# Kernel tuning notes

Measured on AMD Instinct MI355X. Metric: run time of the kernel, lower is better.

## Reference

```python
import jax, jax.numpy as jnp
import numpy as np

N_E = 16384
E_DIM = 64
GROUPS = 4
N_E_GROUP = N_E // GROUPS  # 4096
B, H, W = 16, 32, 32


def _l2norm(x):
    # matches F.normalize(p=2, dim=-1) with eps=1e-12
    n = jnp.linalg.norm(x, axis=-1, keepdims=True)
    return x / jnp.maximum(n, 1e-12)


def setup_inputs() -> dict:
    key = jax.random.key(0)
    k1, k2 = jax.random.split(key)
    z_groups = jax.random.normal(k1, (B, GROUPS * E_DIM, H, W), dtype=jnp.float32)
    emb = jax.random.uniform(k2, (N_E, E_DIM), minval=-1.0 / N_E, maxval=1.0 / N_E,
                             dtype=jnp.float32)
    emb = _l2norm(emb)  # module normalizes codebook at init when l2_norm=True
    return {"z_groups": z_groups, "embedding": emb}


def reference(z_groups, embedding):
    # Eval-mode forward (no EMA/random-restart buffer updates, losses are 0).
    b, c, h, w = z_groups.shape
    # split channels into groups: b (g*c) h w -> b h w g c
    z = z_groups.reshape(b, GROUPS, E_DIM, h, w).transpose(0, 3, 4, 1, 2)
    z = _l2norm(z)                                     # l2_norm=True path
    zf = z.reshape(-1, GROUPS, E_DIM)                  # [N, g, c]
    emb = _l2norm(embedding.reshape(GROUPS, N_E_GROUP, E_DIM))  # [g, k, c]

    # d = -|z|^2 - |e|^2 + 2 z.e  (negative squared distance), argmax = nearest
    d = (2.0 * jnp.einsum('ngc,gkc->ngk', zf, emb)
         - jnp.sum(zf * zf, axis=-1)[..., None]
         - jnp.sum(emb * emb, axis=-1)[None, :, :])    # [N, g, k]
    idx = jnp.argmax(d, axis=-1)                       # [N, g]

    zq = emb[jnp.arange(GROUPS)[None, :], idx]         # [N, g, c] gather
    zq = zf + jax.lax.stop_gradient(zq - zf)           # straight-through

    # b h w g c -> b (g*c) h w
    quant = zq.reshape(b, h, w, GROUPS, E_DIM).transpose(0, 3, 4, 1, 2)
    quant = quant.reshape(b, GROUPS * E_DIM, h, w)

    vq_loss = jnp.zeros((GROUPS,), jnp.float32)
    commit_loss = jnp.zeros((GROUPS,), jnp.float32)
    codebook_usage = jnp.zeros((GROUPS,), jnp.float32)

    # perplexity / min_encodings correspond to the last group (loop semantics)
    min_encodings = jax.nn.one_hot(idx[:, -1], N_E_GROUP, dtype=quant.dtype)
    avg_probs = jnp.mean(min_encodings, axis=0)
    perplexity = jnp.exp(-jnp.sum(avg_probs * jnp.log(avg_probs + 1e-10)))

    return (quant, vq_loss, commit_loss, codebook_usage,
            perplexity, min_encodings, idx)
```

## Files before the change

kernel.cpp:

```cpp
#include <hip/hip_runtime.h>
#include <hip/hip_bf16.h>
#include <math.h>

#define N_E      16384
#define E_DIM    64
#define GROUPS   4
#define N_E_G    4096
#define NQ       16384

#define OFF_QUANT   0L
#define OFF_VQLOSS  4194304L
#define OFF_PERP    4194316L
#define OFF_MINENC  4194317L
#define OFF_IDX     71303181L

#define WS_EN     0L
#define WS_EN2    1048576L
#define WS_ENHI   1064960L
#define WS_HIST   7880704L
#define WS_IDX3   7884800L

typedef float  float4v  __attribute__((ext_vector_type(4)));
typedef short  short8   __attribute__((ext_vector_type(8)));

static __device__ __forceinline__ ushort f2bf(float x) {
    union { __hip_bfloat16 h; ushort u; } cv; cv.h = __float2bfloat16(x);
    return cv.u;
}

__global__ void norm_emb_kernel(const float* __restrict__ emb,
                                float* __restrict__ en, float* __restrict__ en2,
                                ushort* __restrict__ ehi,
                                int* __restrict__ hist) {
    const int t    = threadIdx.x;
    const int lane = t & 63;
    const int wv   = t >> 6;

    if (blockIdx.x < 16) hist[blockIdx.x * 256 + t] = 0;

    #pragma unroll
    for (int it = 0; it < 4; ++it) {
        int code = blockIdx.x * 16 + wv * 4 + it;
        float x = emb[code * 64 + lane];
        float ss = x * x;
        #pragma unroll
        for (int off = 32; off; off >>= 1) ss += __shfl_xor(ss, off, 64);
        float v = x / fmaxf(sqrtf(ss), 1e-12f);
        en[code * 64 + lane]  = v;
        ehi[code * 64 + lane] = f2bf(v);
        float s2 = v * v;
        #pragma unroll
        for (int off = 32; off; off >>= 1) s2 += __shfl_xor(s2, off, 64);
        if (lane == 0) en2[code] = s2;
    }
}

#define CAP  64
#define TAU  0.017f
#define ZSTR 68

__global__ __launch_bounds__(256, 2)
void vq_cand_kernel(const float* __restrict__ z,
                    const ushort* __restrict__ ehi,
                    const float* __restrict__ en,
                    const float* __restrict__ en2, float* __restrict__ out,
                    int* __restrict__ hist, int* __restrict__ idx3) {
    __shared__ float zn[128 * ZSTR];
    __shared__ float rden[128];
    __shared__ union {
        float tile[64 * 129];
        struct {
            ushort cand[128 * CAP];
            int    cnt[128];
            int    bks[128];
        } kl;
    } sh;

    const int g  = blockIdx.y;
    const int q0 = blockIdx.x * 128;
    const int t  = threadIdx.x;
    const int wave = t >> 6, lane = t & 63;
    const int l15 = lane & 15, quad = lane >> 4;
    const int qhalf = wave & 1, chalf = wave >> 1;

    const int sliceId = blockIdx.y * (NQ / 128) + blockIdx.x;
    float4v* fill4 = (float4v*)(out + OFF_VQLOSS) + (size_t)sliceId * 32768;

    const ushort* abase = ehi + (size_t)g * N_E_G * 64
                        + (size_t)(chalf * 64 + l15) * 64 + quad * 8;
    short8 afA[4][2], afB[4][2];
    #pragma unroll
    for (int cs = 0; cs < 4; ++cs)
        #pragma unroll
        for (int ks = 0; ks < 2; ++ks)
            afA[cs][ks] = *(const short8*)(abase + (size_t)(cs * 16) * 64 + ks * 32);

    {
        const int b = q0 >> 10, hw0 = q0 & 1023;
        const float* src = z + (size_t)b * 262144 + (size_t)g * 65536 + hw0;
        for (int i = t; i < 8192; i += 256) {
            int d = i >> 7, nq = i & 127;
            sh.tile[d * 129 + nq] = src[(size_t)d * 1024 + nq];
        }
        __syncthreads();
        if (t < 128) {
            float ss = 0.f;
            for (int d = 0; d < 64; ++d) {
                float x = sh.tile[d * 129 + t];
                ss = fmaf(x, x, ss);
            }
            rden[t] = fmaxf(sqrtf(ss), 1e-12f);
        }
        __syncthreads();
        for (int i = t; i < 8192; i += 256) {
            int q = i >> 6, d = i & 63;
            zn[q * ZSTR + d] = sh.tile[d * 129 + q] / rden[q];
        }
        __syncthreads();
    }

    if (t < 128) sh.kl.cnt[t] = 0;

    short8 bfrag[4][2];
    #pragma unroll
    for (int uu = 0; uu < 4; ++uu) {
        int ql = qhalf * 64 + uu * 16 + l15;
        #pragma unroll
        for (int ks = 0; ks < 2; ++ks) {
            const float* p = &zn[ql * ZSTR + ks * 32 + quad * 8];
            float4v a = *(const float4v*)p;
            float4v c = *(const float4v*)(p + 4);
            short8 f;
            f[0] = (short)f2bf(a[0]); f[1] = (short)f2bf(a[1]);
            f[2] = (short)f2bf(a[2]); f[3] = (short)f2bf(a[3]);
            f[4] = (short)f2bf(c[0]); f[5] = (short)f2bf(c[1]);
            f[6] = (short)f2bf(c[2]); f[7] = (short)f2bf(c[3]);
            bfrag[uu][ks] = f;
        }
    }
    __syncthreads();

    float Mrun[4];
    #pragma unroll
    for (int u = 0; u < 4; ++u) Mrun[u] = -3.4e38f;

    auto do_tile = [&](short8 (&A)[4][2], short8 (&P)[4][2], int tile) {
        if (tile + 1 < 32) {
            const ushort* p = abase + (size_t)((tile + 1) * 128) * 64;
            #pragma unroll
            for (int cs = 0; cs < 4; ++cs)
                #pragma unroll
                for (int ks = 0; ks < 2; ++ks)
                    P[cs][ks] = *(const short8*)(p + (size_t)(cs * 16) * 64 + ks * 32);
        }
        {
            const float4v z4 = {0.f, 0.f, 0.f, 0.f};
            #pragma unroll
            for (int r = 0; r < 4; ++r)
                __builtin_nontemporal_store(
                    z4, &fill4[(size_t)(tile * 4 + r) * 256 + t]);
        }
        float4v acc[4][4];
        #pragma unroll
        for (int cs = 0; cs < 4; ++cs)
            #pragma unroll
            for (int u = 0; u < 4; ++u) {
                float4v zz = {0.f, 0.f, 0.f, 0.f};
                float4v tmp = __builtin_amdgcn_mfma_f32_16x16x32_bf16(
                                  A[cs][0], bfrag[u][0], zz, 0, 0, 0);
                acc[cs][u] = __builtin_amdgcn_mfma_f32_16x16x32_bf16(
                                  A[cs][1], bfrag[u][1], tmp, 0, 0, 0);
            }
        const int j0 = tile * 128;
        #pragma unroll
        for (int u = 0; u < 4; ++u) {
            float m0 = fmaxf(fmaxf(acc[0][u][0], acc[0][u][1]),
                             fmaxf(acc[0][u][2], acc[0][u][3]));
            float m1 = fmaxf(fmaxf(acc[1][u][0], acc[1][u][1]),
                             fmaxf(acc[1][u][2], acc[1][u][3]));
            float m2 = fmaxf(fmaxf(acc[2][u][0], acc[2][u][1]),
                             fmaxf(acc[2][u][2], acc[2][u][3]));
            float m3 = fmaxf(fmaxf(acc[3][u][0], acc[3][u][1]),
                             fmaxf(acc[3][u][2], acc[3][u][3]));
            float m  = fmaxf(fmaxf(m0, m1), fmaxf(m2, m3));
            float mh = fmaxf(m,  __shfl_xor(m,  16, 64));
            float mw = fmaxf(mh, __shfl_xor(mh, 32, 64));
            Mrun[u] = fmaxf(Mrun[u], mw);
            float thr = Mrun[u] - TAU;
            if (m >= thr) {
                int ql = qhalf * 64 + u * 16 + l15;
                #pragma unroll
                for (int cs = 0; cs < 4; ++cs)
                    #pragma unroll
                    for (int r = 0; r < 4; ++r)
                        if (acc[cs][u][r] >= thr) {
                            int cidx = j0 + chalf * 64 + cs * 16 + quad * 4 + r;
                            int slot = atomicAdd(&sh.kl.cnt[ql], 1);
                            if (slot < CAP) sh.kl.cand[ql * CAP + slot] = (ushort)cidx;
                        }
            }
        }
    };

    for (int tt = 0; tt < 32; tt += 2) {
        do_tile(afA, afB, tt);
        do_tile(afB, afA, tt + 1);
    }

    if (sliceId == 0 && t < 13) out[OFF_VQLOSS + 67108864L + t] = 0.f;
    __syncthreads();

    if (t < 128) {
        int q = q0 + t;
        float za[64];
        const float4v* zp = (const float4v*)(&zn[t * ZSTR]);
        #pragma unroll
        for (int i = 0; i < 16; ++i) {
            float4v v = zp[i];
            za[i*4+0] = v[0]; za[i*4+1] = v[1]; za[i*4+2] = v[2]; za[i*4+3] = v[3];
        }
        int nc = sh.kl.cnt[t]; if (nc > CAP) nc = CAP;
        float best = -3.4e38f; int bk = 0x7fffffff;
        for (int s = 0; s < nc; ++s) {
            int c = sh.kl.cand[t * CAP + s];
            const float* ev = en + ((size_t)g * N_E_G + c) * 64;
            float a = 0.f;
            #pragma unroll
            for (int k = 0; k < 64; ++k) a = fmaf(za[k], ev[k], a);
            float d = 2.f * a - en2[g * N_E_G + c];
            if (d > best || (d == best && c < bk)) { best = d; bk = c; }
        }
        if (bk == 0x7fffffff) bk = 0;
        sh.kl.bks[t] = bk;
        out[OFF_IDX + (size_t)q * 4 + g] = (float)bk;
        if (g == 3) {
            idx3[q] = bk;
            atomicAdd(&hist[bk], 1);
        }
    }
    __syncthreads();

    for (int i = t; i < 128 * 64; i += 256) {
        int d = i >> 7, m = i & 127;
        int n = q0 + m, b = n >> 10, hw = n & 1023;
        float v = en[((size_t)g * N_E_G + sh.kl.bks[m]) * 64 + d];
        __builtin_nontemporal_store(
            v, &out[OFF_QUANT + (size_t)b * 262144 + (size_t)(g * 64 + d) * 1024 + hw]);
    }
}

__global__ void finalize_kernel(const int* __restrict__ idx3,
                                const int* __restrict__ hist,
                                float* __restrict__ out) {
    if (blockIdx.x < 64) {
        int r = blockIdx.x * 256 + threadIdx.x;
        out[OFF_MINENC + (size_t)r * N_E_G + idx3[r]] = 1.0f;
        return;
    }
    __shared__ float s[256];
    int t = threadIdx.x;
    float acc = 0.f;
    for (int k = t; k < N_E_G; k += 256) {
        float p = (float)hist[k] * (1.0f / 16384.0f);
        acc += p * logf(p + 1e-10f);
    }
    s[t] = acc;
    __syncthreads();
    for (int o = 128; o; o >>= 1) {
        if (t < o) s[t] += s[t + o];
        __syncthreads();
    }
    if (t == 0) out[OFF_PERP] = expf(-s[0]);
}

extern "C" void kernel_launch(void* const* d_in, const int* in_sizes, int n_in,
                              void* d_out, int out_size, void* d_ws, size_t ws_size,
                              hipStream_t stream) {
    const float* z_groups = (const float*)d_in[0];
    const float* emb      = (const float*)d_in[1];
    float* out = (float*)d_out;
    float* ws  = (float*)d_ws;

    float*  en   = ws + WS_EN;
    float*  en2  = ws + WS_EN2;
    ushort* ehi  = (ushort*)(ws + WS_ENHI);
    int*    hist = (int*)(ws + WS_HIST);
    int*    idx3 = (int*)(ws + WS_IDX3);

    norm_emb_kernel<<<1024, 256, 0, stream>>>(emb, en, en2, ehi, hist);

    vq_cand_kernel<<<dim3(NQ / 128, GROUPS), 256, 0, stream>>>(
        z_groups, ehi, en, en2, out, hist, idx3);

    finalize_kernel<<<65, 256, 0, stream>>>(idx3, hist, out);
}
```

Measured before the change: 388.9 us.

## Double block size to 512 threads and split candidate rescoring across four slices

Raises the candidate kernel to 512 threads (8 waves), so each wave covers 32 codes per tile instead of 64, which halves the per-wave MFMA accumulators and A-fragment registers. The fp32 rescoring of candidates is split into four strided slices per query, followed by a shared-memory reduction, so more threads work on that serial tail. The intent is higher occupancy and less idle time in the exact-scoring phase. The cost is an extra barrier and extra shared memory, and a launch bound of 4 blocks of 512 may force register spills.

```diff
diff --git a/kernel.cpp b/kernel.cpp
--- a/kernel.cpp
+++ b/kernel.cpp
@@ -59,7 +59,7 @@
 #define TAU  0.017f
 #define ZSTR 68
 
-__global__ __launch_bounds__(256, 2)
+__global__ __launch_bounds__(512, 4)
 void vq_cand_kernel(const float* __restrict__ z,
                     const ushort* __restrict__ ehi,
                     const float* __restrict__ en,
@@ -73,6 +73,8 @@
             ushort cand[128 * CAP];
             int    cnt[128];
             int    bks[128];
+            float  bestd[512];
+            int    bestk[512];
         } kl;
     } sh;
 
@@ -81,16 +83,16 @@
     const int t  = threadIdx.x;
     const int wave = t >> 6, lane = t & 63;
     const int l15 = lane & 15, quad = lane >> 4;
-    const int qhalf = wave & 1, chalf = wave >> 1;
+    const int qhalf = wave & 1, cquad = wave >> 1;
 
     const int sliceId = blockIdx.y * (NQ / 128) + blockIdx.x;
     float4v* fill4 = (float4v*)(out + OFF_VQLOSS) + (size_t)sliceId * 32768;
 
     const ushort* abase = ehi + (size_t)g * N_E_G * 64
-                        + (size_t)(chalf * 64 + l15) * 64 + quad * 8;
-    short8 afA[4][2], afB[4][2];
+                        + (size_t)(cquad * 32 + l15) * 64 + quad * 8;
+    short8 afA[2][2], afB[2][2];
     #pragma unroll
-    for (int cs = 0; cs < 4; ++cs)
+    for (int cs = 0; cs < 2; ++cs)
         #pragma unroll
         for (int ks = 0; ks < 2; ++ks)
             afA[cs][ks] = *(const short8*)(abase + (size_t)(cs * 16) * 64 + ks * 32);
@@ -98,7 +100,7 @@
     {
         const int b = q0 >> 10, hw0 = q0 & 1023;
         const float* src = z + (size_t)b * 262144 + (size_t)g * 65536 + hw0;
-        for (int i = t; i < 8192; i += 256) {
+        for (int i = t; i < 8192; i += 512) {
             int d = i >> 7, nq = i & 127;
             sh.tile[d * 129 + nq] = src[(size_t)d * 1024 + nq];
         }
@@ -112,7 +114,7 @@
             rden[t] = fmaxf(sqrtf(ss), 1e-12f);
         }
         __syncthreads();
-        for (int i = t; i < 8192; i += 256) {
+        for (int i = t; i < 8192; i += 512) {
             int q = i >> 6, d = i & 63;
             zn[q * ZSTR + d] = sh.tile[d * 129 + q] / rden[q];
         }
@@ -144,11 +146,11 @@
     #pragma unroll
     for (int u = 0; u < 4; ++u) Mrun[u] = -3.4e38f;
 
-    auto do_tile = [&](short8 (&A)[4][2], short8 (&P)[4][2], int tile) {
+    auto do_tile = [&](short8 (&A)[2][2], short8 (&P)[2][2], int tile) {
         if (tile + 1 < 32) {
             const ushort* p = abase + (size_t)((tile + 1) * 128) * 64;
             #pragma unroll
-            for (int cs = 0; cs < 4; ++cs)
+            for (int cs = 0; cs < 2; ++cs)
                 #pragma unroll
                 for (int ks = 0; ks < 2; ++ks)
                     P[cs][ks] = *(const short8*)(p + (size_t)(cs * 16) * 64 + ks * 32);
@@ -156,13 +158,13 @@
         {
             const float4v z4 = {0.f, 0.f, 0.f, 0.f};
             #pragma unroll
-            for (int r = 0; r < 4; ++r)
+            for (int r = 0; r < 2; ++r)
                 __builtin_nontemporal_store(
-                    z4, &fill4[(size_t)(tile * 4 + r) * 256 + t]);
-        }
-        float4v acc[4][4];
-        #pragma unroll
-        for (int cs = 0; cs < 4; ++cs)
+                    z4, &fill4[(size_t)(tile * 2 + r) * 512 + t]);
+        }
+        float4v acc[2][4];
+        #pragma unroll
+        for (int cs = 0; cs < 2; ++cs)
             #pragma unroll
             for (int u = 0; u < 4; ++u) {
                 float4v zz = {0.f, 0.f, 0.f, 0.f};
@@ -178,11 +180,7 @@
                              fmaxf(acc[0][u][2], acc[0][u][3]));
             float m1 = fmaxf(fmaxf(acc[1][u][0], acc[1][u][1]),
                              fmaxf(acc[1][u][2], acc[1][u][3]));
-            float m2 = fmaxf(fmaxf(acc[2][u][0], acc[2][u][1]),
-                             fmaxf(acc[2][u][2], acc[2][u][3]));
-            float m3 = fmaxf(fmaxf(acc[3][u][0], acc[3][u][1]),
-                             fmaxf(acc[3][u][2], acc[3][u][3]));
-            float m  = fmaxf(fmaxf(m0, m1), fmaxf(m2, m3));
+            float m  = fmaxf(m0, m1);
             float mh = fmaxf(m,  __shfl_xor(m,  16, 64));
             float mw = fmaxf(mh, __shfl_xor(mh, 32, 64));
             Mrun[u] = fmaxf(Mrun[u], mw);
@@ -190,11 +188,11 @@
             if (m >= thr) {
                 int ql = qhalf * 64 + u * 16 + l15;
                 #pragma unroll
-                for (int cs = 0; cs < 4; ++cs)
+                for (int cs = 0; cs < 2; ++cs)
                     #pragma unroll
                     for (int r = 0; r < 4; ++r)
                         if (acc[cs][u][r] >= thr) {
-                            int cidx = j0 + chalf * 64 + cs * 16 + quad * 4 + r;
+                            int cidx = j0 + cquad * 32 + cs * 16 + quad * 4 + r;
                             int slot = atomicAdd(&sh.kl.cnt[ql], 1);
                             if (slot < CAP) sh.kl.cand[ql * CAP + slot] = (ushort)cidx;
                         }
@@ -210,19 +208,19 @@
     if (sliceId == 0 && t < 13) out[OFF_VQLOSS + 67108864L + t] = 0.f;
     __syncthreads();
 
-    if (t < 128) {
-        int q = q0 + t;
+    {
+        int ql = t & 127, slice = t >> 7;
         float za[64];
-        const float4v* zp = (const float4v*)(&zn[t * ZSTR]);
+        const float4v* zp = (const float4v*)(&zn[ql * ZSTR]);
         #pragma unroll
         for (int i = 0; i < 16; ++i) {
             float4v v = zp[i];
             za[i*4+0] = v[0]; za[i*4+1] = v[1]; za[i*4+2] = v[2]; za[i*4+3] = v[3];
         }
-        int nc = sh.kl.cnt[t]; if (nc > CAP) nc = CAP;
+        int nc = sh.kl.cnt[ql]; if (nc > CAP) nc = CAP;
         float best = -3.4e38f; int bk = 0x7fffffff;
-        for (int s = 0; s < nc; ++s) {
-            int c = sh.kl.cand[t * CAP + s];
+        for (int s = slice; s < nc; s += 4) {
+            int c = sh.kl.cand[ql * CAP + s];
             const float* ev = en + ((size_t)g * N_E_G + c) * 64;
             float a = 0.f;
             #pragma unroll
@@ -230,17 +228,30 @@
             float d = 2.f * a - en2[g * N_E_G + c];
             if (d > best || (d == best && c < bk)) { best = d; bk = c; }
         }
+        sh.kl.bestd[t] = best;
+        sh.kl.bestk[t] = bk;
+    }
+    __syncthreads();
+
+    if (t < 128) {
+        float best = -3.4e38f; int bk = 0x7fffffff;
+        #pragma unroll
+        for (int sl = 0; sl < 4; ++sl) {
+            float d = sh.kl.bestd[sl * 128 + t];
+            int   c = sh.kl.bestk[sl * 128 + t];
+            if (d > best || (d == best && c < bk)) { best = d; bk = c; }
+        }
         if (bk == 0x7fffffff) bk = 0;
         sh.kl.bks[t] = bk;
-        out[OFF_IDX + (size_t)q * 4 + g] = (float)bk;
+        out[OFF_IDX + (size_t)(q0 + t) * 4 + g] = (float)bk;
         if (g == 3) {
-            idx3[q] = bk;
+            idx3[q0 + t] = bk;
             atomicAdd(&hist[bk], 1);
         }
     }
     __syncthreads();
 
-    for (int i = t; i < 128 * 64; i += 256) {
+    for (int i = t; i < 128 * 64; i += 512) {
         int d = i >> 7, m = i & 127;
         int n = q0 + m, b = n >> 10, hw = n & 1023;
         float v = en[((size_t)g * N_E_G + sh.kl.bks[m]) * 64 + d];
@@ -289,7 +300,7 @@
 
     norm_emb_kernel<<<1024, 256, 0, stream>>>(emb, en, en2, ehi, hist);
 
-    vq_cand_kernel<<<dim3(NQ / 128, GROUPS), 256, 0, stream>>>(
+    vq_cand_kernel<<<dim3(NQ / 128, GROUPS), 512, 0, stream>>>(
         z_groups, ehi, en, en2, out, hist, idx3);
 
     finalize_kernel<<<65, 256, 0, stream>>>(idx3, hist, out);
```

Result: slower. 402.9 us (+3.6%).

## Split candidate generation and exact rescoring into separate kernels

Applied to the files above, without the earlier changes.

The fused VQ kernel is split into a candidate-generation kernel, which writes per-query candidate lists and counts to workspace, and a separate rescoring kernel, which reloads z, recomputes the norms and does the fp32 exact search and quantized output write. The zn shared buffer is removed and the bf16 fragments are built straight from the transposed tile, so shared memory drops and launch bounds rise from 2 to 4 blocks per SM. The goal is higher occupancy for the MFMA scan and less register and LDS pressure in each phase. In exchange z is read twice, candidates go through global memory, and there is one more launch.

```diff
diff --git a/kernel.cpp b/kernel.cpp
--- a/kernel.cpp
+++ b/kernel.cpp
@@ -17,8 +17,10 @@
 #define WS_EN     0L
 #define WS_EN2    1048576L
 #define WS_ENHI   1064960L
-#define WS_HIST   7880704L
-#define WS_IDX3   7884800L
+#define WS_CAND   1589248L
+#define WS_CNT    3686400L
+#define WS_HIST   3751936L
+#define WS_IDX3   3756032L
 
 typedef float  float4v  __attribute__((ext_vector_type(4)));
 typedef short  short8   __attribute__((ext_vector_type(8)));
@@ -57,23 +59,17 @@
 
 #define CAP  64
 #define TAU  0.017f
-#define ZSTR 68
-
-__global__ __launch_bounds__(256, 2)
-void vq_cand_kernel(const float* __restrict__ z,
-                    const ushort* __restrict__ ehi,
-                    const float* __restrict__ en,
-                    const float* __restrict__ en2, float* __restrict__ out,
-                    int* __restrict__ hist, int* __restrict__ idx3) {
-    __shared__ float zn[128 * ZSTR];
+
+__global__ __launch_bounds__(256, 4)
+void cand_gen_kernel(const float* __restrict__ z,
+                     const ushort* __restrict__ ehi,
+                     float* __restrict__ out,
+                     ushort* __restrict__ candw, int* __restrict__ cntw) {
     __shared__ float rden[128];
+    __shared__ int   cnt[128];
     __shared__ union {
-        float tile[64 * 129];
-        struct {
-            ushort cand[128 * CAP];
-            int    cnt[128];
-            int    bks[128];
-        } kl;
+        float  tile[64 * 129];
+        ushort cand[128 * CAP];
     } sh;
 
     const int g  = blockIdx.y;
@@ -83,7 +79,7 @@
     const int l15 = lane & 15, quad = lane >> 4;
     const int qhalf = wave & 1, chalf = wave >> 1;
 
-    const int sliceId = blockIdx.y * (NQ / 128) + blockIdx.x;
+    const int sliceId = blockIdx.y * 128 + blockIdx.x;
     float4v* fill4 = (float4v*)(out + OFF_VQLOSS) + (size_t)sliceId * 32768;
 
     const ushort* abase = ehi + (size_t)g * N_E_G * 64
@@ -94,6 +90,8 @@
         #pragma unroll
         for (int ks = 0; ks < 2; ++ks)
             afA[cs][ks] = *(const short8*)(abase + (size_t)(cs * 16) * 64 + ks * 32);
+
+    if (t < 128) cnt[t] = 0;
 
     {
         const int b = q0 >> 10, hw0 = q0 & 1023;
@@ -112,29 +110,21 @@
             rden[t] = fmaxf(sqrtf(ss), 1e-12f);
         }
         __syncthreads();
-        for (int i = t; i < 8192; i += 256) {
-            int q = i >> 6, d = i & 63;
-            zn[q * ZSTR + d] = sh.tile[d * 129 + q] / rden[q];
-        }
-        __syncthreads();
-    }
-
-    if (t < 128) sh.kl.cnt[t] = 0;
+    }
 
     short8 bfrag[4][2];
     #pragma unroll
     for (int uu = 0; uu < 4; ++uu) {
         int ql = qhalf * 64 + uu * 16 + l15;
+        float rr = rden[ql];
         #pragma unroll
         for (int ks = 0; ks < 2; ++ks) {
-            const float* p = &zn[ql * ZSTR + ks * 32 + quad * 8];
-            float4v a = *(const float4v*)p;
-            float4v c = *(const float4v*)(p + 4);
             short8 f;
-            f[0] = (short)f2bf(a[0]); f[1] = (short)f2bf(a[1]);
-            f[2] = (short)f2bf(a[2]); f[3] = (short)f2bf(a[3]);
-            f[4] = (short)f2bf(c[0]); f[5] = (short)f2bf(c[1]);
-            f[6] = (short)f2bf(c[2]); f[7] = (short)f2bf(c[3]);
+            #pragma unroll
+            for (int j = 0; j < 8; ++j) {
+                int col = ks * 32 + quad * 8 + j;
+                f[j] = (short)f2bf(sh.tile[col * 129 + ql] / rr);
+            }
             bfrag[uu][ks] = f;
         }
     }
@@ -195,8 +185,8 @@
                     for (int r = 0; r < 4; ++r)
                         if (acc[cs][u][r] >= thr) {
                             int cidx = j0 + chalf * 64 + cs * 16 + quad * 4 + r;
-                            int slot = atomicAdd(&sh.kl.cnt[ql], 1);
-                            if (slot < CAP) sh.kl.cand[ql * CAP + slot] = (ushort)cidx;
+                            int slot = atomicAdd(&cnt[ql], 1);
+                            if (slot < CAP) sh.cand[ql * CAP + slot] = (ushort)cidx;
                         }
             }
         }
@@ -210,19 +200,63 @@
     if (sliceId == 0 && t < 13) out[OFF_VQLOSS + 67108864L + t] = 0.f;
     __syncthreads();
 
+    {
+        const uint* s  = (const uint*)sh.cand;
+        uint* d2 = (uint*)(candw + (size_t)sliceId * 128 * CAP);
+        for (int i = t; i < 128 * CAP / 2; i += 256) d2[i] = s[i];
+    }
     if (t < 128) {
-        int q = q0 + t;
+        int n = cnt[t];
+        cntw[sliceId * 128 + t] = n > CAP ? CAP : n;
+    }
+}
+
+__global__ __launch_bounds__(256, 4)
+void rescore_kernel(const float* __restrict__ z,
+                    const float* __restrict__ en,
+                    const float* __restrict__ en2,
+                    const ushort* __restrict__ candw,
+                    const int* __restrict__ cntw,
+                    float* __restrict__ out,
+                    int* __restrict__ hist, int* __restrict__ idx3) {
+    __shared__ float tile[64 * 129];
+    __shared__ float rden[128];
+    __shared__ int   bks[128];
+
+    const int g  = blockIdx.y;
+    const int q0 = blockIdx.x * 128;
+    const int t  = threadIdx.x;
+    const int sliceId = blockIdx.y * 128 + blockIdx.x;
+
+    {
+        const int b = q0 >> 10, hw0 = q0 & 1023;
+        const float* src = z + (size_t)b * 262144 + (size_t)g * 65536 + hw0;
+        for (int i = t; i < 8192; i += 256) {
+            int d = i >> 7, nq = i & 127;
+            tile[d * 129 + nq] = src[(size_t)d * 1024 + nq];
+        }
+        __syncthreads();
+        if (t < 128) {
+            float ss = 0.f;
+            for (int d = 0; d < 64; ++d) {
+                float x = tile[d * 129 + t];
+                ss = fmaf(x, x, ss);
+            }
+            rden[t] = fmaxf(sqrtf(ss), 1e-12f);
+        }
+        __syncthreads();
+    }
+
+    if (t < 128) {
+        float rr = rden[t];
         float za[64];
-        const float4v* zp = (const float4v*)(&zn[t * ZSTR]);
-        #pragma unroll
-        for (int i = 0; i < 16; ++i) {
-            float4v v = zp[i];
-            za[i*4+0] = v[0]; za[i*4+1] = v[1]; za[i*4+2] = v[2]; za[i*4+3] = v[3];
-        }
-        int nc = sh.kl.cnt[t]; if (nc > CAP) nc = CAP;
+        #pragma unroll
+        for (int k = 0; k < 64; ++k) za[k] = tile[k * 129 + t] / rr;
+        int nc = cntw[sliceId * 128 + t];
+        const ushort* cr = candw + (size_t)sliceId * 128 * CAP + t * CAP;
         float best = -3.4e38f; int bk = 0x7fffffff;
         for (int s = 0; s < nc; ++s) {
-            int c = sh.kl.cand[t * CAP + s];
+            int c = cr[s];
             const float* ev = en + ((size_t)g * N_E_G + c) * 64;
             float a = 0.f;
             #pragma unroll
@@ -231,10 +265,10 @@
             if (d > best || (d == best && c < bk)) { best = d; bk = c; }
         }
         if (bk == 0x7fffffff) bk = 0;
-        sh.kl.bks[t] = bk;
-        out[OFF_IDX + (size_t)q * 4 + g] = (float)bk;
+        bks[t] = bk;
+        out[OFF_IDX + (size_t)(q0 + t) * 4 + g] = (float)bk;
         if (g == 3) {
-            idx3[q] = bk;
+            idx3[q0 + t] = bk;
             atomicAdd(&hist[bk], 1);
         }
     }
@@ -243,7 +277,7 @@
     for (int i = t; i < 128 * 64; i += 256) {
         int d = i >> 7, m = i & 127;
         int n = q0 + m, b = n >> 10, hw = n & 1023;
-        float v = en[((size_t)g * N_E_G + sh.kl.bks[m]) * 64 + d];
+        float v = en[((size_t)g * N_E_G + bks[m]) * 64 + d];
         __builtin_nontemporal_store(
             v, &out[OFF_QUANT + (size_t)b * 262144 + (size_t)(g * 64 + d) * 1024 + hw]);
     }
@@ -284,13 +318,18 @@
     float*  en   = ws + WS_EN;
     float*  en2  = ws + WS_EN2;
     ushort* ehi  = (ushort*)(ws + WS_ENHI);
+    ushort* candw= (ushort*)(ws + WS_CAND);
+    int*    cntw = (int*)(ws + WS_CNT);
     int*    hist = (int*)(ws + WS_HIST);
     int*    idx3 = (int*)(ws + WS_IDX3);
 
     norm_emb_kernel<<<1024, 256, 0, stream>>>(emb, en, en2, ehi, hist);
 
-    vq_cand_kernel<<<dim3(NQ / 128, GROUPS), 256, 0, stream>>>(
-        z_groups, ehi, en, en2, out, hist, idx3);
+    cand_gen_kernel<<<dim3(NQ / 128, GROUPS), 256, 0, stream>>>(
+        z_groups, ehi, out, candw, cntw);
+
+    rescore_kernel<<<dim3(NQ / 128, GROUPS), 256, 0, stream>>>(
+        z_groups, en, en2, candw, cntw, out, hist, idx3);
 
     finalize_kernel<<<65, 256, 0, stream>>>(idx3, hist, out);
 }
```

After: 605.5 us. +55.7%, slower.
